# Optimization experiments

Hardware: AMD Instinct MI355X
Metric: run time of the kernel (lower is better)

Reference implementation:

```python
import jax, jax.numpy as jnp
import numpy as np

N = 50000        # num nodes
E = 1600000      # num edges (before self loops)
F_IN = 128
F_OUT = 64
SLOPE = 0.2      # PyG GATConv default negative_slope


def setup_inputs() -> dict:
    key = jax.random.key(0)
    k0, k1, k2, k3, k4, k5 = jax.random.split(key, 6)
    x = jax.random.normal(k0, (N, F_IN), dtype=jnp.float32)
    # GATConv params (heads=1): linear weight, attention vectors, bias
    W = jax.random.normal(k1, (F_IN, F_OUT), dtype=jnp.float32) * (1.0 / np.sqrt(F_IN))
    a_src = jax.random.normal(k2, (F_OUT,), dtype=jnp.float32) * (1.0 / np.sqrt(F_OUT))
    a_dst = jax.random.normal(k3, (F_OUT,), dtype=jnp.float32) * (1.0 / np.sqrt(F_OUT))
    bias = jax.random.normal(k4, (F_OUT,), dtype=jnp.float32) * 0.01
    edge_index = jax.random.randint(k5, (2, E), 0, N, dtype=jnp.int32)
    return {"x": x, "W": W, "a_src": a_src, "a_dst": a_dst, "bias": bias,
            "edge_index": edge_index}


def reference(x, W, a_src, a_dst, bias, edge_index):
    # Linear transform: [N, F_OUT]
    xp = x @ W
    # add self loops (PyG GATConv default add_self_loops=True)
    loop = jnp.arange(N, dtype=edge_index.dtype)
    src = jnp.concatenate([edge_index[0], loop])  # source j of edge j->i
    dst = jnp.concatenate([edge_index[1], loop])  # target i
    # per-node attention logits, gathered per edge
    alpha_s = xp @ a_src  # [N]
    alpha_d = xp @ a_dst  # [N]
    e = alpha_s[src] + alpha_d[dst]               # [E+N]
    e = jnp.where(e > 0, e, SLOPE * e)            # leaky_relu(0.2)
    # segment softmax over edges grouped by destination node
    emax = jax.ops.segment_max(e, dst, num_segments=N)  # every node has a self loop
    w = jnp.exp(e - emax[dst])
    denom = jax.ops.segment_sum(w, dst, num_segments=N)
    alpha = w / denom[dst]                        # [E+N]
    # scatter-aggregate weighted source features
    out = jax.ops.segment_sum(alpha[:, None] * xp[src], dst, num_segments=N)
    out = out + bias
    # F.relu then unsqueeze(dim=0) and cat with empty -> [1, N, F_OUT]
    return jax.nn.relu(out)[None, :, :]
```

## Files before the change

kernel.cpp:

```cpp
#include <hip/hip_runtime.h>
#include <hip/hip_fp16.h>
#include <math.h>

#define N_NODES 50000
#define N_EDGES 1600000
#define ET (N_EDGES + N_NODES)
#define F_OUT 64
#define F_IN 128
#define SLOPE 0.2f
#define BSHIFT 7
#define BNODES 128
#define NBUCK ((N_NODES + BNODES - 1) >> BSHIFT)
#define CAP 4736
#define EPB 4096
#define PBLOCKS ((ET + EPB - 1) / EPB)

typedef _Float16 half8 __attribute__((ext_vector_type(8)));
typedef _Float16 half4 __attribute__((ext_vector_type(4)));
typedef float f32x4 __attribute__((ext_vector_type(4)));

__global__ __launch_bounds__(256) void gemm_kernel(const float4* __restrict__ x4,
                                                   const float4* __restrict__ W4,
                                                   const float* __restrict__ a_src,
                                                   const float* __restrict__ a_dst,
                                                   _Float16* __restrict__ xph,
                                                   float* __restrict__ alpha_s,
                                                   float* __restrict__ alpha_d,
                                                   int* __restrict__ bcur) {
    __shared__ _Float16 xs[64][136];
    __shared__ float    Wsh[F_IN * F_OUT];
    int t = threadIdx.x;
    if (blockIdx.x == 0)
        for (int i = t; i < NBUCK; i += 256) bcur[i] = 0;
    int wave = t >> 6, lane = t & 63;
    int g = lane >> 4, c16 = lane & 15;

#pragma unroll
    for (int i = 0; i < 8; ++i)
        ((float4*)Wsh)[t + i * 256] = W4[t + i * 256];
    size_t rbase = (size_t)blockIdx.x * 64;
#pragma unroll
    for (int i = 0; i < 8; ++i) {
        int idx = t + i * 256;
        int row = idx >> 5, c4 = idx & 31;
        size_t gr = rbase + row;
        if (gr >= N_NODES) gr = N_NODES - 1;
        float4 v = x4[gr * (F_IN / 4) + c4];
        half4 hv = { (_Float16)v.x, (_Float16)v.y, (_Float16)v.z, (_Float16)v.w };
        *(half4*)&xs[row][c4 * 4] = hv;
    }
    __syncthreads();

    half8 bw[4][4];
#pragma unroll
    for (int nt = 0; nt < 4; ++nt)
#pragma unroll
        for (int kt = 0; kt < 4; ++kt) {
            int col = nt * 16 + c16;
            int k0 = kt * 32 + g * 8;
#pragma unroll
            for (int e = 0; e < 8; ++e)
                bw[nt][kt][e] = (_Float16)Wsh[(k0 + e) * F_OUT + col];
        }

    int r0 = wave * 16;
    half8 af[4];
#pragma unroll
    for (int kt = 0; kt < 4; ++kt)
        af[kt] = *(const half8*)&xs[r0 + c16][kt * 32 + g * 8];

    f32x4 acc[4];
#pragma unroll
    for (int nt = 0; nt < 4; ++nt) {
        acc[nt] = (f32x4){0.f, 0.f, 0.f, 0.f};
#pragma unroll
        for (int kt = 0; kt < 4; ++kt)
            acc[nt] = __builtin_amdgcn_mfma_f32_16x16x32_f16(af[kt], bw[nt][kt], acc[nt], 0, 0, 0);
    }

    int growbase = (int)rbase + r0 + g * 4;
#pragma unroll
    for (int nt = 0; nt < 4; ++nt) {
#pragma unroll
        for (int r = 0; r < 4; ++r) {
            int row = growbase + r;
            if (row < N_NODES)
                xph[(size_t)row * F_OUT + nt * 16 + c16] = (_Float16)acc[nt][r];
        }
    }
    float asl[4], adl[4];
#pragma unroll
    for (int nt = 0; nt < 4; ++nt) {
        asl[nt] = a_src[nt * 16 + c16];
        adl[nt] = a_dst[nt * 16 + c16];
    }
#pragma unroll
    for (int r = 0; r < 4; ++r) {
        float ps = 0.f, pd = 0.f;
#pragma unroll
        for (int nt = 0; nt < 4; ++nt) {
            ps = fmaf(acc[nt][r], asl[nt], ps);
            pd = fmaf(acc[nt][r], adl[nt], pd);
        }
#pragma unroll
        for (int off = 1; off < 16; off <<= 1) {
            ps += __shfl_xor(ps, off);
            pd += __shfl_xor(pd, off);
        }
        int row = growbase + r;
        if (c16 == 0 && row < N_NODES) { alpha_s[row] = ps; alpha_d[row] = pd; }
    }
}

__global__ __launch_bounds__(256) void part_kernel(const int* __restrict__ ei,
                                                   int* __restrict__ bcur,
                                                   unsigned* __restrict__ rec) {
    __shared__ int lc[NBUCK];
    __shared__ int lbase[NBUCK];
    int t = threadIdx.x;
    for (int b = t; b < NBUCK; b += 256) lc[b] = 0;
    __syncthreads();
    int e0 = blockIdx.x * EPB;

    unsigned u[16]; short bk[16]; unsigned short rk[16];
#pragma unroll
    for (int k = 0; k < 4; ++k) {
        int e = e0 + k * 1024 + t * 4;
        int4 sv, dv;
        if (e + 3 < N_EDGES) {
            sv = *(const int4*)&ei[e];
            dv = *(const int4*)&ei[N_EDGES + e];
        } else {
            int* sp = (int*)&sv; int* dp = (int*)&dv;
#pragma unroll
            for (int j = 0; j < 4; ++j) {
                int ee = e + j;
                if (ee < N_EDGES)      { sp[j] = ei[ee]; dp[j] = ei[N_EDGES + ee]; }
                else if (ee < ET)      { sp[j] = dp[j] = ee - N_EDGES; }
                else                   { sp[j] = dp[j] = -1; }
            }
        }
        const int* sp = (const int*)&sv; const int* dp = (const int*)&dv;
#pragma unroll
        for (int j = 0; j < 4; ++j) {
            int i = k * 4 + j;
            int d = dp[j];
            if (d >= 0) {
                int b = d >> BSHIFT;
                bk[i] = (short)b;
                rk[i] = (unsigned short)atomicAdd(&lc[b], 1);
                u[i] = (unsigned)sp[j] | ((unsigned)d << 16);
            } else bk[i] = -1;
        }
    }
    __syncthreads();
    for (int b = t; b < NBUCK; b += 256)
        lbase[b] = lc[b] ? (b * CAP + atomicAdd(&bcur[b], lc[b])) : 0;
    __syncthreads();
#pragma unroll
    for (int i = 0; i < 16; ++i)
        if (bk[i] >= 0) rec[lbase[bk[i]] + rk[i]] = u[i];
}

__device__ __forceinline__ int block_incl_scan(int v, int t, int* wsum) {
    int lane = t & 63, wave = t >> 6;
#pragma unroll
    for (int off = 1; off < 64; off <<= 1) {
        int n = __shfl_up(v, off);
        if (lane >= off) v += n;
    }
    if (lane == 63) wsum[wave] = v;
    __syncthreads();
    int add = 0;
    for (int w = 0; w < wave; ++w) add += wsum[w];
    return v + add;
}

__global__ __launch_bounds__(512) void csrb_kernel(const unsigned* __restrict__ rec,
                                                   const int* __restrict__ bcur,
                                                   const float* __restrict__ as,
                                                   const float* __restrict__ ad,
                                                   int* __restrict__ offsets,
                                                   int* __restrict__ counts,
                                                   unsigned* __restrict__ wcsr) {
    __shared__ unsigned lrec[CAP];
    __shared__ int lcnt[BNODES], loff[BNODES], lcur[BNODES];
    __shared__ float adl[BNODES];
    __shared__ int wsum[8];
    int t = threadIdx.x;
    int b = blockIdx.x;
    int n0 = b << BSHIFT;
    int r0 = b * CAP;
    int cnt_b = bcur[b];
    if (t < BNODES) {
        lcnt[t] = 0; lcur[t] = 0;
        adl[t] = (n0 + t < N_NODES) ? ad[n0 + t] : 0.f;
    }
    for (int i = t; i < cnt_b; i += 512) lrec[i] = rec[r0 + i];
    __syncthreads();
    for (int i = t; i < cnt_b; i += 512)
        atomicAdd(&lcnt[(lrec[i] >> 16) & (BNODES - 1)], 1);
    __syncthreads();
    int v = (t < BNODES) ? lcnt[t] : 0;
    int incl = block_incl_scan(v, t, wsum);
    if (t < BNODES) {
        loff[t] = incl - v;
        if (n0 + t < N_NODES) { counts[n0 + t] = v; offsets[n0 + t] = r0 + incl - v; }
    }
    __syncthreads();
    for (int i = t; i < cnt_b; i += 512) {
        unsigned u = lrec[i];
        int dl = (u >> 16) & (BNODES - 1);
        int s = u & 0xFFFFu;
        float ev = as[s] + adl[dl];
        ev = ev > 0.f ? ev : SLOPE * ev;
        float w = __expf(ev);
        int pos = atomicAdd(&lcur[dl], 1);
        wcsr[r0 + loff[dl] + pos] =
            (unsigned)s | ((unsigned)__half_as_ushort(__float2half(w)) << 16);
    }
}

__global__ __launch_bounds__(256) void gather_kernel(const unsigned* __restrict__ wcsr,
                                                     const int* __restrict__ offsets,
                                                     const int* __restrict__ counts,
                                                     const __half* __restrict__ xp,
                                                     const float* __restrict__ bias,
                                                     float* __restrict__ out) {
    __shared__ unsigned stage[4][64];
    int wave = threadIdx.x >> 6, lane = threadIdx.x & 63;
    int d = blockIdx.x * 4 + wave;
    if (d >= N_NODES) return;
    int start = offsets[d], cnt = counts[d];
    int q = lane >> 4, f = lane & 15;
    const uint2* xp2 = (const uint2*)xp;
    float4 acc = make_float4(0.f, 0.f, 0.f, 0.f);
    float ws = 0.f;

    for (int jb = 0; jb < cnt; jb += 64) {
        int iters = min(cnt - jb, 64);
        unsigned rc = (lane < iters) ? wcsr[start + jb + lane] : 0u;
        stage[wave][lane] = rc;
        int m = (iters - q + 3) >> 2;
        unsigned u = stage[wave][q];
        uint2 hv = xp2[(u & 0xFFFFu) * 16 + f];
        for (int i = 0; i < m; ++i) {
            unsigned u_cur = u;
            uint2 hv_cur = hv;
            if (i + 1 < m) {
                u = stage[wave][q + (i + 1) * 4];
                hv = xp2[(u & 0xFFFFu) * 16 + f];
            }
            float w = __half2float(__ushort_as_half((unsigned short)(u_cur >> 16)));
            __half2 h0 = __builtin_bit_cast(__half2, hv_cur.x);
            __half2 h1 = __builtin_bit_cast(__half2, hv_cur.y);
            float2 f0 = __half22float2(h0);
            float2 f1 = __half22float2(h1);
            acc.x = fmaf(w, f0.x, acc.x);
            acc.y = fmaf(w, f0.y, acc.y);
            acc.z = fmaf(w, f1.x, acc.z);
            acc.w = fmaf(w, f1.y, acc.w);
            ws += w;
        }
    }
#pragma unroll
    for (int off = 16; off < 64; off <<= 1) {
        acc.x += __shfl_xor(acc.x, off);
        acc.y += __shfl_xor(acc.y, off);
        acc.z += __shfl_xor(acc.z, off);
        acc.w += __shfl_xor(acc.w, off);
        ws    += __shfl_xor(ws, off);
    }
    if (q == 0) {
        float inv = 1.f / ws;
        float4 bl = ((const float4*)bias)[f];
        float4 o;
        o.x = fmaf(acc.x, inv, bl.x);
        o.y = fmaf(acc.y, inv, bl.y);
        o.z = fmaf(acc.z, inv, bl.z);
        o.w = fmaf(acc.w, inv, bl.w);
        o.x = o.x > 0.f ? o.x : 0.f;
        o.y = o.y > 0.f ? o.y : 0.f;
        o.z = o.z > 0.f ? o.z : 0.f;
        o.w = o.w > 0.f ? o.w : 0.f;
        ((float4*)out)[(size_t)d * 16 + f] = o;
    }
}

extern "C" void kernel_launch(void* const* d_in, const int* in_sizes, int n_in,
                              void* d_out, int out_size, void* d_ws, size_t ws_size,
                              hipStream_t stream) {
    const float* x     = (const float*)d_in[0];
    const float* W     = (const float*)d_in[1];
    const float* a_src = (const float*)d_in[2];
    const float* a_dst = (const float*)d_in[3];
    const float* bias  = (const float*)d_in[4];
    const int*   ei    = (const int*)d_in[5];
    float* out = (float*)d_out;

    _Float16* xph   = (_Float16*)d_ws;
    float*  as      = (float*)(xph + (size_t)N_NODES * F_OUT);
    float*  ad      = as + N_NODES;
    int*    counts  = (int*)(ad + N_NODES);
    int*    offsets = counts + N_NODES;
    int*    bcur    = offsets + N_NODES;
    unsigned* rec   = (unsigned*)(bcur + NBUCK + 64);
    unsigned* wcsr  = rec + (size_t)NBUCK * CAP;

    gemm_kernel<<<(N_NODES + 63) / 64, 256, 0, stream>>>(
        (const float4*)x, (const float4*)W, a_src, a_dst, xph, as, ad, bcur);
    part_kernel<<<PBLOCKS, 256, 0, stream>>>(ei, bcur, rec);
    csrb_kernel<<<NBUCK, 512, 0, stream>>>(rec, bcur, as, ad, offsets, counts, wcsr);
    gather_kernel<<<(N_NODES + 3) / 4, 256, 0, stream>>>(wcsr, offsets, counts,
                                                         (const __half*)xph, bias, out);
}
```

Baseline: 93.82 us.

## Fuse per-bucket CSR build with gather aggregation and shrink buckets to 64 nodes

Merges the CSR-building kernel and the gather kernel into one bucket kernel. The weighted CSR for each 64-node bucket stays in shared memory, so the global wcsr, offsets and counts round trips and one launch are removed. The gather loop now keeps four loads in flight per lane, and the GEMM reads W directly from global memory instead of staging it in LDS. The trade-offs are lower per-block parallelism, since each wave serially processes 16 destination nodes, and a fixed per-bucket capacity that could overflow on skewed degree distributions.

```diff
diff --git a/kernel.cpp b/kernel.cpp
--- a/kernel.cpp
+++ b/kernel.cpp
@@ -8,10 +8,10 @@
 #define F_OUT 64
 #define F_IN 128
 #define SLOPE 0.2f
-#define BSHIFT 7
-#define BNODES 128
+#define BSHIFT 6
+#define BNODES 64
 #define NBUCK ((N_NODES + BNODES - 1) >> BSHIFT)
-#define CAP 4736
+#define CAP 2496
 #define EPB 4096
 #define PBLOCKS ((ET + EPB - 1) / EPB)
 
@@ -20,7 +20,7 @@
 typedef float f32x4 __attribute__((ext_vector_type(4)));
 
 __global__ __launch_bounds__(256) void gemm_kernel(const float4* __restrict__ x4,
-                                                   const float4* __restrict__ W4,
+                                                   const float* __restrict__ W,
                                                    const float* __restrict__ a_src,
                                                    const float* __restrict__ a_dst,
                                                    _Float16* __restrict__ xph,
@@ -28,16 +28,12 @@
                                                    float* __restrict__ alpha_d,
                                                    int* __restrict__ bcur) {
     __shared__ _Float16 xs[64][136];
-    __shared__ float    Wsh[F_IN * F_OUT];
     int t = threadIdx.x;
     if (blockIdx.x == 0)
         for (int i = t; i < NBUCK; i += 256) bcur[i] = 0;
     int wave = t >> 6, lane = t & 63;
     int g = lane >> 4, c16 = lane & 15;
 
-#pragma unroll
-    for (int i = 0; i < 8; ++i)
-        ((float4*)Wsh)[t + i * 256] = W4[t + i * 256];
     size_t rbase = (size_t)blockIdx.x * 64;
 #pragma unroll
     for (int i = 0; i < 8; ++i) {
@@ -49,7 +45,6 @@
         half4 hv = { (_Float16)v.x, (_Float16)v.y, (_Float16)v.z, (_Float16)v.w };
         *(half4*)&xs[row][c4 * 4] = hv;
     }
-    __syncthreads();
 
     half8 bw[4][4];
 #pragma unroll
@@ -60,8 +55,9 @@
             int k0 = kt * 32 + g * 8;
 #pragma unroll
             for (int e = 0; e < 8; ++e)
-                bw[nt][kt][e] = (_Float16)Wsh[(k0 + e) * F_OUT + col];
-        }
+                bw[nt][kt][e] = (_Float16)W[(k0 + e) * F_OUT + col];
+        }
+    __syncthreads();
 
     int r0 = wave * 16;
     half8 af[4];
@@ -162,31 +158,30 @@
         if (bk[i] >= 0) rec[lbase[bk[i]] + rk[i]] = u[i];
 }
 
-__device__ __forceinline__ int block_incl_scan(int v, int t, int* wsum) {
-    int lane = t & 63, wave = t >> 6;
-#pragma unroll
-    for (int off = 1; off < 64; off <<= 1) {
-        int n = __shfl_up(v, off);
-        if (lane >= off) v += n;
-    }
-    if (lane == 63) wsum[wave] = v;
-    __syncthreads();
-    int add = 0;
-    for (int w = 0; w < wave; ++w) add += wsum[w];
-    return v + add;
-}
-
-__global__ __launch_bounds__(512) void csrb_kernel(const unsigned* __restrict__ rec,
-                                                   const int* __restrict__ bcur,
-                                                   const float* __restrict__ as,
-                                                   const float* __restrict__ ad,
-                                                   int* __restrict__ offsets,
-                                                   int* __restrict__ counts,
-                                                   unsigned* __restrict__ wcsr) {
+__device__ __forceinline__ void consume(unsigned u, uint2 h, bool valid,
+                                        float4& acc, float& ws) {
+    float w = __half2float(__ushort_as_half((unsigned short)(u >> 16)));
+    w = valid ? w : 0.f;
+    float2 f0 = __half22float2(__builtin_bit_cast(__half2, h.x));
+    float2 f1 = __half22float2(__builtin_bit_cast(__half2, h.y));
+    acc.x = fmaf(w, f0.x, acc.x);
+    acc.y = fmaf(w, f0.y, acc.y);
+    acc.z = fmaf(w, f1.x, acc.z);
+    acc.w = fmaf(w, f1.y, acc.w);
+    ws += w;
+}
+
+__global__ __launch_bounds__(256) void bucket_kernel(const unsigned* __restrict__ rec,
+                                                     const int* __restrict__ bcur,
+                                                     const float* __restrict__ as,
+                                                     const float* __restrict__ ad,
+                                                     const __half* __restrict__ xp,
+                                                     const float* __restrict__ bias,
+                                                     float* __restrict__ out) {
     __shared__ unsigned lrec[CAP];
+    __shared__ unsigned lcsr[CAP];
     __shared__ int lcnt[BNODES], loff[BNODES], lcur[BNODES];
     __shared__ float adl[BNODES];
-    __shared__ int wsum[8];
     int t = threadIdx.x;
     int b = blockIdx.x;
     int n0 = b << BSHIFT;
@@ -196,19 +191,25 @@
         lcnt[t] = 0; lcur[t] = 0;
         adl[t] = (n0 + t < N_NODES) ? ad[n0 + t] : 0.f;
     }
-    for (int i = t; i < cnt_b; i += 512) lrec[i] = rec[r0 + i];
-    __syncthreads();
-    for (int i = t; i < cnt_b; i += 512)
-        atomicAdd(&lcnt[(lrec[i] >> 16) & (BNODES - 1)], 1);
-    __syncthreads();
-    int v = (t < BNODES) ? lcnt[t] : 0;
-    int incl = block_incl_scan(v, t, wsum);
+    __syncthreads();
+    for (int i = t; i < cnt_b; i += 256) {
+        unsigned u = rec[r0 + i];
+        lrec[i] = u;
+        atomicAdd(&lcnt[(u >> 16) & (BNODES - 1)], 1);
+    }
+    __syncthreads();
     if (t < BNODES) {
+        int v = lcnt[t];
+        int incl = v;
+#pragma unroll
+        for (int off = 1; off < BNODES; off <<= 1) {
+            int n = __shfl_up(incl, off);
+            if (t >= off) incl += n;
+        }
         loff[t] = incl - v;
-        if (n0 + t < N_NODES) { counts[n0 + t] = v; offsets[n0 + t] = r0 + incl - v; }
-    }
-    __syncthreads();
-    for (int i = t; i < cnt_b; i += 512) {
+    }
+    __syncthreads();
+    for (int i = t; i < cnt_b; i += 256) {
         unsigned u = lrec[i];
         int dl = (u >> 16) & (BNODES - 1);
         int s = u & 0xFFFFu;
@@ -216,74 +217,66 @@
         ev = ev > 0.f ? ev : SLOPE * ev;
         float w = __expf(ev);
         int pos = atomicAdd(&lcur[dl], 1);
-        wcsr[r0 + loff[dl] + pos] =
+        lcsr[loff[dl] + pos] =
             (unsigned)s | ((unsigned)__half_as_ushort(__float2half(w)) << 16);
     }
-}
-
-__global__ __launch_bounds__(256) void gather_kernel(const unsigned* __restrict__ wcsr,
-                                                     const int* __restrict__ offsets,
-                                                     const int* __restrict__ counts,
-                                                     const __half* __restrict__ xp,
-                                                     const float* __restrict__ bias,
-                                                     float* __restrict__ out) {
-    __shared__ unsigned stage[4][64];
-    int wave = threadIdx.x >> 6, lane = threadIdx.x & 63;
-    int d = blockIdx.x * 4 + wave;
-    if (d >= N_NODES) return;
-    int start = offsets[d], cnt = counts[d];
+    __syncthreads();
+    int wave = t >> 6, lane = t & 63;
     int q = lane >> 4, f = lane & 15;
     const uint2* xp2 = (const uint2*)xp;
-    float4 acc = make_float4(0.f, 0.f, 0.f, 0.f);
-    float ws = 0.f;
-
-    for (int jb = 0; jb < cnt; jb += 64) {
-        int iters = min(cnt - jb, 64);
-        unsigned rc = (lane < iters) ? wcsr[start + jb + lane] : 0u;
-        stage[wave][lane] = rc;
-        int m = (iters - q + 3) >> 2;
-        unsigned u = stage[wave][q];
-        uint2 hv = xp2[(u & 0xFFFFu) * 16 + f];
-        for (int i = 0; i < m; ++i) {
-            unsigned u_cur = u;
-            uint2 hv_cur = hv;
-            if (i + 1 < m) {
-                u = stage[wave][q + (i + 1) * 4];
-                hv = xp2[(u & 0xFFFFu) * 16 + f];
-            }
-            float w = __half2float(__ushort_as_half((unsigned short)(u_cur >> 16)));
-            __half2 h0 = __builtin_bit_cast(__half2, hv_cur.x);
-            __half2 h1 = __builtin_bit_cast(__half2, hv_cur.y);
-            float2 f0 = __half22float2(h0);
-            float2 f1 = __half22float2(h1);
-            acc.x = fmaf(w, f0.x, acc.x);
-            acc.y = fmaf(w, f0.y, acc.y);
-            acc.z = fmaf(w, f1.x, acc.z);
-            acc.w = fmaf(w, f1.y, acc.w);
-            ws += w;
-        }
-    }
-#pragma unroll
-    for (int off = 16; off < 64; off <<= 1) {
-        acc.x += __shfl_xor(acc.x, off);
-        acc.y += __shfl_xor(acc.y, off);
-        acc.z += __shfl_xor(acc.z, off);
-        acc.w += __shfl_xor(acc.w, off);
-        ws    += __shfl_xor(ws, off);
-    }
-    if (q == 0) {
-        float inv = 1.f / ws;
-        float4 bl = ((const float4*)bias)[f];
-        float4 o;
-        o.x = fmaf(acc.x, inv, bl.x);
-        o.y = fmaf(acc.y, inv, bl.y);
-        o.z = fmaf(acc.z, inv, bl.z);
-        o.w = fmaf(acc.w, inv, bl.w);
-        o.x = o.x > 0.f ? o.x : 0.f;
-        o.y = o.y > 0.f ? o.y : 0.f;
-        o.z = o.z > 0.f ? o.z : 0.f;
-        o.w = o.w > 0.f ? o.w : 0.f;
-        ((float4*)out)[(size_t)d * 16 + f] = o;
+    for (int j = 0; j < 16; ++j) {
+        int dl = wave * 16 + j;
+        if (n0 + dl >= N_NODES) break;
+        int start = loff[dl], cnt = lcnt[dl];
+        int m = (cnt - q + 3) >> 2;
+        int cm1 = start + cnt - 1;
+        int p0 = start + q;
+        unsigned u0 = lcsr[min(p0, cm1)];
+        unsigned u1 = lcsr[min(p0 + 4, cm1)];
+        unsigned u2 = lcsr[min(p0 + 8, cm1)];
+        unsigned u3 = lcsr[min(p0 + 12, cm1)];
+        uint2 h0 = xp2[(u0 & 0xFFFFu) * 16 + f];
+        uint2 h1 = xp2[(u1 & 0xFFFFu) * 16 + f];
+        uint2 h2 = xp2[(u2 & 0xFFFFu) * 16 + f];
+        uint2 h3 = xp2[(u3 & 0xFFFFu) * 16 + f];
+        float4 acc = make_float4(0.f, 0.f, 0.f, 0.f);
+        float ws = 0.f;
+        for (int i = 0; i < m; i += 4) {
+            consume(u0, h0, true, acc, ws);
+            if (i + 4 < m) { u0 = lcsr[p0 + (i + 4) * 4];
+                             h0 = xp2[(u0 & 0xFFFFu) * 16 + f]; }
+            consume(u1, h1, i + 1 < m, acc, ws);
+            if (i + 5 < m) { u1 = lcsr[p0 + (i + 5) * 4];
+                             h1 = xp2[(u1 & 0xFFFFu) * 16 + f]; }
+            consume(u2, h2, i + 2 < m, acc, ws);
+            if (i + 6 < m) { u2 = lcsr[p0 + (i + 6) * 4];
+                             h2 = xp2[(u2 & 0xFFFFu) * 16 + f]; }
+            consume(u3, h3, i + 3 < m, acc, ws);
+            if (i + 7 < m) { u3 = lcsr[p0 + (i + 7) * 4];
+                             h3 = xp2[(u3 & 0xFFFFu) * 16 + f]; }
+        }
+#pragma unroll
+        for (int off = 16; off < 64; off <<= 1) {
+            acc.x += __shfl_xor(acc.x, off);
+            acc.y += __shfl_xor(acc.y, off);
+            acc.z += __shfl_xor(acc.z, off);
+            acc.w += __shfl_xor(acc.w, off);
+            ws    += __shfl_xor(ws, off);
+        }
+        if (q == 0) {
+            float inv = 1.f / ws;
+            float4 bl = ((const float4*)bias)[f];
+            float4 o;
+            o.x = fmaf(acc.x, inv, bl.x);
+            o.y = fmaf(acc.y, inv, bl.y);
+            o.z = fmaf(acc.z, inv, bl.z);
+            o.w = fmaf(acc.w, inv, bl.w);
+            o.x = o.x > 0.f ? o.x : 0.f;
+            o.y = o.y > 0.f ? o.y : 0.f;
+            o.z = o.z > 0.f ? o.z : 0.f;
+            o.w = o.w > 0.f ? o.w : 0.f;
+            ((float4*)out)[(size_t)(n0 + dl) * 16 + f] = o;
+        }
     }
 }
 
@@ -301,16 +294,12 @@
     _Float16* xph   = (_Float16*)d_ws;
     float*  as      = (float*)(xph + (size_t)N_NODES * F_OUT);
     float*  ad      = as + N_NODES;
-    int*    counts  = (int*)(ad + N_NODES);
-    int*    offsets = counts + N_NODES;
-    int*    bcur    = offsets + N_NODES;
+    int*    bcur    = (int*)(ad + N_NODES);
     unsigned* rec   = (unsigned*)(bcur + NBUCK + 64);
-    unsigned* wcsr  = rec + (size_t)NBUCK * CAP;
 
     gemm_kernel<<<(N_NODES + 63) / 64, 256, 0, stream>>>(
-        (const float4*)x, (const float4*)W, a_src, a_dst, xph, as, ad, bcur);
+        (const float4*)x, W, a_src, a_dst, xph, as, ad, bcur);
     part_kernel<<<PBLOCKS, 256, 0, stream>>>(ei, bcur, rec);
-    csrb_kernel<<<NBUCK, 512, 0, stream>>>(rec, bcur, as, ad, offsets, counts, wcsr);
-    gather_kernel<<<(N_NODES + 3) / 4, 256, 0, stream>>>(wcsr, offsets, counts,
-                                                         (const __half*)xph, bias, out);
-}
+    bucket_kernel<<<NBUCK, 256, 0, stream>>>(rec, bcur, as, ad,
+                                             (const __half*)xph, bias, out);
+}
```

New measurement: 95.53 us. About the same (+1.8%).
